# Kernel tuning notes

Hardware: AMD Instinct MI355X
Metric: run time of the kernel (lower is better)

## Reference

```python
import jax, jax.numpy as jnp
import numpy as np

TOKENS = 16384
IN_F = 2048
OUT_F = 2048
RANK = 32
GROUP = 64          # int4 scale group size
PAD = 256           # token padding multiple used by the fused activation quantizer
QMAX = 7.0          # signed int4 symmetric quantization


def setup_inputs() -> dict:
    key = jax.random.key(0)
    ks = jax.random.split(key, 7)
    x = jax.random.normal(ks[0], (TOKENS, IN_F), dtype=jnp.float32)
    # packed int4 weights: two signed nibbles per int8 lane
    qweight = jax.random.randint(ks[1], (OUT_F, IN_F // 2), -128, 128, dtype=jnp.int8)
    # per-group weight scales [in//group, out], strictly positive
    wscales = jnp.abs(jax.random.normal(ks[2], (IN_F // GROUP, OUT_F), dtype=jnp.float32)) * 0.01 + 1e-4
    # activation smoothing factors, positive and near 1
    smooth_factor = jnp.abs(jax.random.normal(ks[3], (IN_F,), dtype=jnp.float32)) * 0.5 + 0.75
    bias = jax.random.normal(ks[4], (OUT_F,), dtype=jnp.float32) * 0.01
    proj_down = jax.random.normal(ks[5], (IN_F, RANK), dtype=jnp.float32) * 0.02
    proj_up = jax.random.normal(ks[6], (OUT_F, RANK), dtype=jnp.float32) * 0.02
    return {"x": x, "qweight": qweight, "wscales": wscales,
            "smooth_factor": smooth_factor, "bias": bias,
            "proj_down": proj_down, "proj_up": proj_up}


def _unpack_int4(qweight):
    # low nibble = even input channel, high nibble = odd input channel; arithmetic shifts keep sign
    low = jnp.right_shift(jnp.left_shift(qweight, 4), 4)
    high = jnpp = jnp.right_shift(qweight, 4)
    w = jnp.stack([low, high], axis=-1).reshape(qweight.shape[0], qweight.shape[1] * 2)
    return w.astype(jnp.float32)  # [out, in], values in [-8, 7]


def _forward(x, qweight, wscales, smooth_factor, bias, proj_down, proj_up):
    T = x.shape[0]
    t_pad = ((T + PAD - 1) // PAD) * PAD
    # activation smoothing
    xs = x / smooth_factor
    xs_p = jnp.pad(xs, ((0, t_pad - T), (0, 0)))
    # per-token per-64-group symmetric int4 activation quantization
    xg = xs_p.reshape(t_pad, IN_F // GROUP, GROUP)
    amax = jnp.max(jnp.abs(xg), axis=-1)                       # [Tp, G]
    ascales = jnp.where(amax > 0, amax / QMAX, jnp.float32(1.0))
    qx = jnp.clip(jnp.round(xg / ascales[..., None]), -8.0, 7.0)
    xdq = (qx * ascales[..., None]).reshape(t_pad, IN_F)       # dequantized activations
    # dequantize packed int4 weights with per-group scales
    w = _unpack_int4(qweight)                                  # [out, in]
    wdq = (w.reshape(OUT_F, IN_F // GROUP, GROUP) * wscales.T[:, :, None]).reshape(OUT_F, IN_F)
    # packed GEMM (dequantized equivalent) + fused low-rank residual + bias
    y = xdq @ wdq.T                                            # [Tp, out]
    y = y + (xs_p @ proj_down) @ proj_up.T + bias
    return y[:T]


def reference(x, qweight, wscales, smooth_factor, bias, proj_down, proj_up):
    return _forward(x, qweight, wscales, smooth_factor, bias, proj_down, proj_up)
```

## Files before the change

kernel.cpp:

```cpp
#include <hip/hip_runtime.h>

#define TOKENS 16384
#define INF 2048
#define OUTF 2048
#define NGROUP 32
#define RANK 32
#define BM 128
#define BN 128

typedef int   int32x4  __attribute__((ext_vector_type(4)));
typedef int   int32x2  __attribute__((ext_vector_type(2)));
typedef float floatx4  __attribute__((ext_vector_type(4)));
typedef short bf16x8   __attribute__((ext_vector_type(8)));

typedef __attribute__((address_space(1))) const void gconst_t;
typedef __attribute__((address_space(3))) void ldsv_t;

__device__ __forceinline__ void gload_lds16(const void* g, void* l) {
  __builtin_amdgcn_global_load_lds((gconst_t*)g, (ldsv_t*)l, 16, 0, 0);
}

__device__ __forceinline__ unsigned short f2bf(float f) {
  unsigned u = __float_as_uint(f);
  unsigned r = (u + 0x7FFFu + ((u >> 16) & 1u)) >> 16;
  return (unsigned short)r;
}

__device__ __forceinline__ unsigned unp2(int e0, int e1) {
  int l0 = ((int)((unsigned)e0 << 28)) >> 28;
  int h0 = ((int)((unsigned)e0 << 24)) >> 28;
  int l1 = ((int)((unsigned)e1 << 28)) >> 28;
  int h1 = ((int)((unsigned)e1 << 24)) >> 28;
  return (l0 & 0xFF) | ((h0 & 0xFF) << 8) | ((l1 & 0xFF) << 16) | ((h1 & 0xFF) << 24);
}

__global__ __launch_bounds__(256) void unpack_kernel(const int* __restrict__ qw,
                                                     signed char* __restrict__ wq8) {
  int idx = blockIdx.x * 256 + threadIdx.x;
  const int4* src = (const int4*)qw;
  int4 v0 = src[idx * 2 + 0];
  int4 v1 = src[idx * 2 + 1];
  int4 out;
  out.x = (int)unp2(v0.x, v0.y);
  out.y = (int)unp2(v0.z, v0.w);
  out.z = (int)unp2(v1.x, v1.y);
  out.w = (int)unp2(v1.z, v1.w);
  *(int4*)(wq8 + (size_t)idx * 16) = out;
}

__global__ __launch_bounds__(256) void prep_pdT(const float* __restrict__ pd,
                                                unsigned short* __restrict__ pdT) {
  int idx = blockIdx.x * 256 + threadIdx.x;
  int r = idx >> 11, c = idx & 2047;
  pdT[idx] = f2bf(pd[(size_t)c * RANK + r]);
}

__global__ __launch_bounds__(256) void quant_kernel(
    const float* __restrict__ x, const float* __restrict__ smooth,
    const unsigned short* __restrict__ pdT,
    signed char* __restrict__ qx8, float* __restrict__ ascales,
    float* __restrict__ tdown) {
  __shared__ char lds[32768];
  int tid = threadIdx.x, lane = tid & 63, wid = tid >> 6;
  int t0 = blockIdx.x * 32;
  int mi = wid >> 1, ni = wid & 1;
  floatx4 acc = {0.f, 0.f, 0.f, 0.f};

  floatx4 xv[8];
  floatx4 sm;
  int32x4 pv[4];

  auto issue_loads = [&](int kc) {
    const float* xb = x + (size_t)(t0 + wid * 8) * INF + kc * 256 + lane * 4;
#pragma unroll
    for (int r = 0; r < 8; ++r) xv[r] = *(const floatx4*)(xb + r * INF);
    sm = *(const floatx4*)(smooth + kc * 256 + lane * 4);
#pragma unroll
    for (int q = 0; q < 4; ++q) {
      int flat = tid + q * 256;
      int row = flat >> 5, c16 = flat & 31;
      pv[q] = *(const int32x4*)((const char*)pdT + (size_t)row * 4096 + kc * 512 + c16 * 16);
    }
  };

  issue_loads(0);

  for (int kc = 0; kc < 8; ++kc) {
    floatx4 rsm;
    rsm[0] = 1.0f / sm[0]; rsm[1] = 1.0f / sm[1];
    rsm[2] = 1.0f / sm[2]; rsm[3] = 1.0f / sm[3];
#pragma unroll
    for (int q = 0; q < 4; ++q) {
      int flat = tid + q * 256;
      int row = flat >> 5, c16 = flat & 31;
      int byte = (row * 512 + c16 * 16) ^ ((row & 7) << 4);
      *(int32x4*)(lds + 16384 + byte) = pv[q];
    }
#pragma unroll
    for (int r = 0; r < 8; ++r) {
      floatx4 xs;
      xs[0] = xv[r][0] * rsm[0]; xs[1] = xv[r][1] * rsm[1];
      xs[2] = xv[r][2] * rsm[2]; xs[3] = xv[r][3] * rsm[3];
      float m4 = fmaxf(fmaxf(fabsf(xs[0]), fabsf(xs[1])),
                       fmaxf(fabsf(xs[2]), fabsf(xs[3])));
      m4 = fmaxf(m4, __shfl_xor(m4, 1, 64));
      m4 = fmaxf(m4, __shfl_xor(m4, 2, 64));
      m4 = fmaxf(m4, __shfl_xor(m4, 4, 64));
      m4 = fmaxf(m4, __shfl_xor(m4, 8, 64));
      float ascale = m4 > 0.f ? m4 / 7.0f : 1.0f;
      float rq = 1.0f / ascale;
      int tok = t0 + wid * 8 + r;
      if ((lane & 15) == 0)
        ascales[(size_t)tok * NGROUP + kc * 4 + (lane >> 4)] = ascale;
      int pk = 0;
#pragma unroll
      for (int b = 0; b < 4; ++b) {
        float qf = fminf(7.f, fmaxf(-8.f, rintf(xs[b] * rq)));
        pk |= ((int)qf & 0xFF) << (8 * b);
      }
      *(int*)(qx8 + (size_t)tok * INF + kc * 256 + lane * 4) = pk;
      unsigned lo = (unsigned)f2bf(xs[0]) | ((unsigned)f2bf(xs[1]) << 16);
      unsigned hi = (unsigned)f2bf(xs[2]) | ((unsigned)f2bf(xs[3]) << 16);
      int lrow = wid * 8 + r;
      int xbyte = (lrow * 512 + lane * 8) ^ ((lrow & 7) << 4);
      int32x2 wv; wv[0] = (int)lo; wv[1] = (int)hi;
      *(int32x2*)(lds + xbyte) = wv;
    }
    __syncthreads();
    if (kc + 1 < 8) issue_loads(kc + 1);
#pragma unroll
    for (int ks = 0; ks < 8; ++ks) {
      int arow = mi * 16 + (lane & 15);
      int ab = (arow * 512 + ks * 64 + ((lane >> 4) << 4)) ^ ((arow & 7) << 4);
      bf16x8 av = *(const bf16x8*)(lds + ab);
      int brow = ni * 16 + (lane & 15);
      int bb = (brow * 512 + ks * 64 + ((lane >> 4) << 4)) ^ ((brow & 7) << 4);
      bf16x8 bv = *(const bf16x8*)(lds + 16384 + bb);
      acc = __builtin_amdgcn_mfma_f32_16x16x32_bf16(av, bv, acc, 0, 0, 0);
    }
    __syncthreads();
  }

  int trow = t0 + mi * 16 + ((lane >> 4) << 2);
  int col = ni * 16 + (lane & 15);
#pragma unroll
  for (int r = 0; r < 4; ++r)
    tdown[(size_t)(trow + r) * RANK + col] = acc[r];
}

__global__ __launch_bounds__(256, 2) void gemm_kernel(
    const signed char* __restrict__ qx8, const signed char* __restrict__ wq8,
    const float* __restrict__ ascales, const float* __restrict__ wscales,
    const float* __restrict__ tdown, const float* __restrict__ pu,
    const float* __restrict__ bias, float* __restrict__ y) {
  __shared__ char smem[81920];
  float* as_t = (float*)(smem + 49152);
  float* ws_t = (float*)(smem + 65536);

  int tid = threadIdx.x;
  int lane = tid & 63;
  int wid = tid >> 6;
  int wr = wid >> 1, wc = wid & 1;
  int o0 = blockIdx.x * BN;
  int t0 = blockIdx.y * BM;

  {
    int tt = tid >> 1, h = (tid & 1) * 16;
    const float* src = ascales + (size_t)(t0 + tt) * NGROUP + h;
#pragma unroll
    for (int q = 0; q < 4; ++q) {
      float4 v = *(const float4*)(src + q * 4);
      as_t[(h + q * 4 + 0) * BM + tt] = v.x;
      as_t[(h + q * 4 + 1) * BM + tt] = v.y;
      as_t[(h + q * 4 + 2) * BM + tt] = v.z;
      as_t[(h + q * 4 + 3) * BM + tt] = v.w;
    }
    int gg = tid >> 3, cc = (tid & 7) * 16;
    const float* src2 = wscales + (size_t)gg * OUTF + o0 + cc;
#pragma unroll
    for (int q = 0; q < 4; ++q)
      *(float4*)&ws_t[gg * BN + cc + q * 4] = *(const float4*)(src2 + q * 4);
  }

  float acc[4][4][4];
#pragma unroll
  for (int m = 0; m < 4; ++m)
#pragma unroll
    for (int n = 0; n < 4; ++n)
#pragma unroll
      for (int r = 0; r < 4; ++r) acc[m][n][r] = 0.f;

  auto stage = [&](int g) {
    int bufb = (g % 3) * 16384;
#pragma unroll
    for (int i = 0; i < 2; ++i) {
      int c = tid + i * 256;
      int row = c >> 2;
      int l = (c & 3) ^ ((row >> 1) & 3);
      gload_lds16(qx8 + (size_t)(t0 + row) * INF + g * 64 + l * 16,
                  smem + bufb + (wid + i * 4) * 1024);
      gload_lds16(wq8 + (size_t)(o0 + row) * INF + g * 64 + l * 16,
                  smem + bufb + 8192 + (wid + i * 4) * 1024);
    }
  };

  int aoff[4], boff[4];
#pragma unroll
  for (int m = 0; m < 4; ++m) {
    int arow = (wr << 6) + (m << 4) + (lane & 15);
    aoff[m] = arow * 64 + ((((lane >> 4)) ^ ((arow >> 1) & 3)) << 4);
    int brow = (wc << 6) + (m << 4) + (lane & 15);
    boff[m] = 8192 + brow * 64 + ((((lane >> 4)) ^ ((brow >> 1) & 3)) << 4);
  }
  int asoff = (wr << 6) + ((lane >> 4) << 2);
  int wsoff = (wc << 6) + (lane & 15);

  __syncthreads();
  stage(0);
  stage(1);

  for (int g = 0; g < NGROUP; ++g) {
    if (g == NGROUP - 1) asm volatile("s_waitcnt vmcnt(0)" ::: "memory");
    else                 asm volatile("s_waitcnt vmcnt(4)" ::: "memory");
    __builtin_amdgcn_s_barrier();
    __builtin_amdgcn_sched_barrier(0);

    if (g + 2 < NGROUP) stage(g + 2);

    int bufb = (g % 3) * 16384;
    int32x4 af[4], bf_[4];
#pragma unroll
    for (int m = 0; m < 4; ++m) af[m] = *(const int32x4*)(smem + bufb + aoff[m]);
#pragma unroll
    for (int n = 0; n < 4; ++n) bf_[n] = *(const int32x4*)(smem + bufb + boff[n]);

    float asv[4][4];
#pragma unroll
    for (int m = 0; m < 4; ++m) {
      floatx4 v = *(const floatx4*)&as_t[g * BM + asoff + (m << 4)];
      asv[m][0] = v[0]; asv[m][1] = v[1]; asv[m][2] = v[2]; asv[m][3] = v[3];
    }
    float wsv[4];
#pragma unroll
    for (int n = 0; n < 4; ++n) wsv[n] = ws_t[g * BN + wsoff + (n << 4)];

    __builtin_amdgcn_s_setprio(1);
#pragma unroll
    for (int m = 0; m < 4; ++m)
#pragma unroll
      for (int n = 0; n < 4; ++n) {
        int32x4 zero = {0, 0, 0, 0};
        int32x4 d = __builtin_amdgcn_mfma_i32_16x16x64_i8(af[m], bf_[n], zero, 0, 0, 0);
#pragma unroll
        for (int r = 0; r < 4; ++r)
          acc[m][n][r] += ((float)d[r] * wsv[n]) * asv[m][r];
      }
    __builtin_amdgcn_s_setprio(0);
  }

  __syncthreads();

  unsigned short* td_lds = (unsigned short*)smem;
  unsigned short* pu_lds = (unsigned short*)(smem + 8192);
  {
    int row = tid >> 1, h = (tid & 1) * 16;
    const float* ts = tdown + (size_t)(t0 + row) * RANK + h;
    const float* ps = pu + (size_t)(o0 + row) * RANK + h;
    unsigned tw[8], pw[8];
#pragma unroll
    for (int q = 0; q < 4; ++q) {
      float4 v = *(const float4*)(ts + q * 4);
      tw[q * 2 + 0] = (unsigned)f2bf(v.x) | ((unsigned)f2bf(v.y) << 16);
      tw[q * 2 + 1] = (unsigned)f2bf(v.z) | ((unsigned)f2bf(v.w) << 16);
      float4 p = *(const float4*)(ps + q * 4);
      pw[q * 2 + 0] = (unsigned)f2bf(p.x) | ((unsigned)f2bf(p.y) << 16);
      pw[q * 2 + 1] = (unsigned)f2bf(p.z) | ((unsigned)f2bf(p.w) << 16);
    }
    int4 s0, s1;
    s0.x = (int)tw[0]; s0.y = (int)tw[1]; s0.z = (int)tw[2]; s0.w = (int)tw[3];
    s1.x = (int)tw[4]; s1.y = (int)tw[5]; s1.z = (int)tw[6]; s1.w = (int)tw[7];
    *(int4*)(td_lds + row * 32 + h) = s0;
    *(int4*)(td_lds + row * 32 + h + 8) = s1;
    s0.x = (int)pw[0]; s0.y = (int)pw[1]; s0.z = (int)pw[2]; s0.w = (int)pw[3];
    s1.x = (int)pw[4]; s1.y = (int)pw[5]; s1.z = (int)pw[6]; s1.w = (int)pw[7];
    *(int4*)(pu_lds + row * 32 + h) = s0;
    *(int4*)(pu_lds + row * 32 + h + 8) = s1;
  }
  __syncthreads();

  bf16x8 ta[4], pb4[4];
  int koff8 = (lane >> 4) << 3;
#pragma unroll
  for (int m = 0; m < 4; ++m)
    ta[m] = *(const bf16x8*)&td_lds[((wr << 6) + (m << 4) + (lane & 15)) * 32 + koff8];
#pragma unroll
  for (int n = 0; n < 4; ++n)
    pb4[n] = *(const bf16x8*)&pu_lds[((wc << 6) + (n << 4) + (lane & 15)) * 32 + koff8];

#pragma unroll
  for (int n = 0; n < 4; ++n) {
    int oc = o0 + (wc << 6) + (n << 4) + (lane & 15);
    float bv = bias[oc];
#pragma unroll
    for (int m = 0; m < 4; ++m) {
      floatx4 c;
      c[0] = acc[m][n][0]; c[1] = acc[m][n][1]; c[2] = acc[m][n][2]; c[3] = acc[m][n][3];
      c = __builtin_amdgcn_mfma_f32_16x16x32_bf16(ta[m], pb4[n], c, 0, 0, 0);
#pragma unroll
      for (int r = 0; r < 4; ++r) {
        int tr = t0 + (wr << 6) + (m << 4) + ((lane >> 4) << 2) + r;
        y[(size_t)tr * OUTF + oc] = c[r] + bv;
      }
    }
  }
}

extern "C" void kernel_launch(void* const* d_in, const int* in_sizes, int n_in,
                              void* d_out, int out_size, void* d_ws, size_t ws_size,
                              hipStream_t stream) {
  const float* x      = (const float*)d_in[0];
  const int*   qw     = (const int*)d_in[1];
  const float* wsc    = (const float*)d_in[2];
  const float* smooth = (const float*)d_in[3];
  const float* bias   = (const float*)d_in[4];
  const float* pd     = (const float*)d_in[5];
  const float* pu     = (const float*)d_in[6];
  float* y = (float*)d_out;

  char* ws = (char*)d_ws;
  signed char* qx8 = (signed char*)ws;
  signed char* wq8 = (signed char*)(ws + 33554432);
  float* ascales   = (float*)(ws + 33554432 + 4194304);
  float* tdown     = (float*)(ws + 33554432 + 4194304 + 2097152);
  unsigned short* pdT = (unsigned short*)((char*)d_out + (64u << 20));

  unpack_kernel<<<1024, 256, 0, stream>>>(qw, wq8);
  prep_pdT<<<256, 256, 0, stream>>>(pd, pdT);
  quant_kernel<<<TOKENS / 32, 256, 0, stream>>>(x, smooth, pdT, qx8, ascales, tdown);
  gemm_kernel<<<dim3(OUTF / BN, TOKENS / BM), 256, 0, stream>>>(
      qx8, wq8, ascales, wsc, tdown, pu, bias, y);
}
```

Before: 206.6 us.

## Prefetch per-group scales into registers, drop LDS scale tables, raise occupancy

The activation scales are now written transposed (group-major) by the quantizer, so the GEMM can load each group's scales straight from global memory into registers one iteration ahead instead of staging whole scale tables in LDS. This cuts GEMM shared memory from 80KB to 48KB, and launch bounds are raised to allow three blocks per CU. The waitcnt thresholds are adjusted for the extra outstanding loads, and the scale multiply is written as vector ops. The risks are higher register pressure at three blocks per CU, and the hand-tuned vmcnt values must exactly match the number of outstanding loads.

```diff
diff --git a/kernel.cpp b/kernel.cpp
--- a/kernel.cpp
+++ b/kernel.cpp
@@ -58,7 +58,7 @@
 __global__ __launch_bounds__(256) void quant_kernel(
     const float* __restrict__ x, const float* __restrict__ smooth,
     const unsigned short* __restrict__ pdT,
-    signed char* __restrict__ qx8, float* __restrict__ ascales,
+    signed char* __restrict__ qx8, float* __restrict__ ascalesT,
     float* __restrict__ tdown) {
   __shared__ char lds[32768];
   int tid = threadIdx.x, lane = tid & 63, wid = tid >> 6;
@@ -111,7 +111,7 @@
       float rq = 1.0f / ascale;
       int tok = t0 + wid * 8 + r;
       if ((lane & 15) == 0)
-        ascales[(size_t)tok * NGROUP + kc * 4 + (lane >> 4)] = ascale;
+        ascalesT[(size_t)(kc * 4 + (lane >> 4)) * TOKENS + tok] = ascale;
       int pk = 0;
 #pragma unroll
       for (int b = 0; b < 4; ++b) {
@@ -148,14 +148,12 @@
     tdown[(size_t)(trow + r) * RANK + col] = acc[r];
 }
 
-__global__ __launch_bounds__(256, 2) void gemm_kernel(
+__global__ __launch_bounds__(256, 3) void gemm_kernel(
     const signed char* __restrict__ qx8, const signed char* __restrict__ wq8,
-    const float* __restrict__ ascales, const float* __restrict__ wscales,
+    const float* __restrict__ ascalesT, const float* __restrict__ wscales,
     const float* __restrict__ tdown, const float* __restrict__ pu,
     const float* __restrict__ bias, float* __restrict__ y) {
-  __shared__ char smem[81920];
-  float* as_t = (float*)(smem + 49152);
-  float* ws_t = (float*)(smem + 65536);
+  __shared__ char smem[49152];
 
   int tid = threadIdx.x;
   int lane = tid & 63;
@@ -164,31 +162,11 @@
   int o0 = blockIdx.x * BN;
   int t0 = blockIdx.y * BM;
 
-  {
-    int tt = tid >> 1, h = (tid & 1) * 16;
-    const float* src = ascales + (size_t)(t0 + tt) * NGROUP + h;
-#pragma unroll
-    for (int q = 0; q < 4; ++q) {
-      float4 v = *(const float4*)(src + q * 4);
-      as_t[(h + q * 4 + 0) * BM + tt] = v.x;
-      as_t[(h + q * 4 + 1) * BM + tt] = v.y;
-      as_t[(h + q * 4 + 2) * BM + tt] = v.z;
-      as_t[(h + q * 4 + 3) * BM + tt] = v.w;
-    }
-    int gg = tid >> 3, cc = (tid & 7) * 16;
-    const float* src2 = wscales + (size_t)gg * OUTF + o0 + cc;
-#pragma unroll
-    for (int q = 0; q < 4; ++q)
-      *(float4*)&ws_t[gg * BN + cc + q * 4] = *(const float4*)(src2 + q * 4);
-  }
-
-  float acc[4][4][4];
+  floatx4 acc[4][4];
 #pragma unroll
   for (int m = 0; m < 4; ++m)
 #pragma unroll
-    for (int n = 0; n < 4; ++n)
-#pragma unroll
-      for (int r = 0; r < 4; ++r) acc[m][n][r] = 0.f;
+    for (int n = 0; n < 4; ++n) acc[m][n] = (floatx4){0.f, 0.f, 0.f, 0.f};
 
   auto stage = [&](int g) {
     int bufb = (g % 3) * 16384;
@@ -212,19 +190,40 @@
     int brow = (wc << 6) + (m << 4) + (lane & 15);
     boff[m] = 8192 + brow * 64 + ((((lane >> 4)) ^ ((brow >> 1) & 3)) << 4);
   }
-  int asoff = (wr << 6) + ((lane >> 4) << 2);
-  int wsoff = (wc << 6) + (lane & 15);
-
-  __syncthreads();
+
+  const float* asp = ascalesT + t0 + (wr << 6) + ((lane >> 4) << 2);
+  const float* wsp = wscales + o0 + (wc << 6) + (lane & 15);
+
+  floatx4 asv_pf[4];
+  float wsv_pf[4];
+  auto scales_pf = [&](int g) {
+#pragma unroll
+    for (int m = 0; m < 4; ++m)
+      asv_pf[m] = *(const floatx4*)(asp + (size_t)g * TOKENS + (m << 4));
+#pragma unroll
+    for (int n = 0; n < 4; ++n)
+      wsv_pf[n] = wsp[(size_t)g * OUTF + (n << 4)];
+  };
+
+  scales_pf(0);
   stage(0);
   stage(1);
 
   for (int g = 0; g < NGROUP; ++g) {
-    if (g == NGROUP - 1) asm volatile("s_waitcnt vmcnt(0)" ::: "memory");
-    else                 asm volatile("s_waitcnt vmcnt(4)" ::: "memory");
+    if (g == 0)               asm volatile("s_waitcnt vmcnt(4)" ::: "memory");
+    else if (g == NGROUP - 1) asm volatile("s_waitcnt vmcnt(8)" ::: "memory");
+    else                      asm volatile("s_waitcnt vmcnt(12)" ::: "memory");
     __builtin_amdgcn_s_barrier();
     __builtin_amdgcn_sched_barrier(0);
 
+    floatx4 asv[4];
+    float wsv[4];
+#pragma unroll
+    for (int m = 0; m < 4; ++m) asv[m] = asv_pf[m];
+#pragma unroll
+    for (int n = 0; n < 4; ++n) wsv[n] = wsv_pf[n];
+
+    if (g + 1 < NGROUP) scales_pf(g + 1);
     if (g + 2 < NGROUP) stage(g + 2);
 
     int bufb = (g % 3) * 16384;
@@ -233,16 +232,6 @@
     for (int m = 0; m < 4; ++m) af[m] = *(const int32x4*)(smem + bufb + aoff[m]);
 #pragma unroll
     for (int n = 0; n < 4; ++n) bf_[n] = *(const int32x4*)(smem + bufb + boff[n]);
-
-    float asv[4][4];
-#pragma unroll
-    for (int m = 0; m < 4; ++m) {
-      floatx4 v = *(const floatx4*)&as_t[g * BM + asoff + (m << 4)];
-      asv[m][0] = v[0]; asv[m][1] = v[1]; asv[m][2] = v[2]; asv[m][3] = v[3];
-    }
-    float wsv[4];
-#pragma unroll
-    for (int n = 0; n < 4; ++n) wsv[n] = ws_t[g * BN + wsoff + (n << 4)];
 
     __builtin_amdgcn_s_setprio(1);
 #pragma unroll
@@ -251,9 +240,10 @@
       for (int n = 0; n < 4; ++n) {
         int32x4 zero = {0, 0, 0, 0};
         int32x4 d = __builtin_amdgcn_mfma_i32_16x16x64_i8(af[m], bf_[n], zero, 0, 0, 0);
-#pragma unroll
-        for (int r = 0; r < 4; ++r)
-          acc[m][n][r] += ((float)d[r] * wsv[n]) * asv[m][r];
+        floatx4 sc;
+        sc[0] = asv[m][0] * wsv[n]; sc[1] = asv[m][1] * wsv[n];
+        sc[2] = asv[m][2] * wsv[n]; sc[3] = asv[m][3] * wsv[n];
+        acc[m][n] += __builtin_convertvector(d, floatx4) * sc;
       }
     __builtin_amdgcn_s_setprio(0);
   }
@@ -303,8 +293,7 @@
     float bv = bias[oc];
 #pragma unroll
     for (int m = 0; m < 4; ++m) {
-      floatx4 c;
-      c[0] = acc[m][n][0]; c[1] = acc[m][n][1]; c[2] = acc[m][n][2]; c[3] = acc[m][n][3];
+      floatx4 c = acc[m][n];
       c = __builtin_amdgcn_mfma_f32_16x16x32_bf16(ta[m], pb4[n], c, 0, 0, 0);
 #pragma unroll
       for (int r = 0; r < 4; ++r) {
@@ -330,13 +319,13 @@
   char* ws = (char*)d_ws;
   signed char* qx8 = (signed char*)ws;
   signed char* wq8 = (signed char*)(ws + 33554432);
-  float* ascales   = (float*)(ws + 33554432 + 4194304);
+  float* ascalesT  = (float*)(ws + 33554432 + 4194304);
   float* tdown     = (float*)(ws + 33554432 + 4194304 + 2097152);
   unsigned short* pdT = (unsigned short*)((char*)d_out + (64u << 20));
 
   unpack_kernel<<<1024, 256, 0, stream>>>(qw, wq8);
   prep_pdT<<<256, 256, 0, stream>>>(pd, pdT);
-  quant_kernel<<<TOKENS / 32, 256, 0, stream>>>(x, smooth, pdT, qx8, ascales, tdown);
+  quant_kernel<<<TOKENS / 32, 256, 0, stream>>>(x, smooth, pdT, qx8, ascalesT, tdown);
   gemm_kernel<<<dim3(OUTF / BN, TOKENS / BM), 256, 0, stream>>>(
-      qx8, wq8, ascales, wsc, tdown, pu, bias, y);
-}
+      qx8, wq8, ascalesT, wsc, tdown, pu, bias, y);
+}
```

Result: slower. 218.9 us (+6.0%).
